# Performance work log

Measured on AMD Instinct MI355X. Metric: run time of the kernel, lower is better.

Reference implementation:

```python
import jax, jax.numpy as jnp
import numpy as np

EPS = 1e-5
K = 20

def knn_idx(x, k):
    # x: (B, C, N); returns indices of k nearest neighbors (incl. self), (B, N, k)
    xx = jnp.sum(x * x, axis=1, keepdims=True)            # (B,1,N)
    inner = -2.0 * jnp.einsum('bcn,bcm->bnm', x, x)       # (B,N,N)
    d = -jnp.swapaxes(xx, 1, 2) - inner - xx              # -||xi - xj||^2
    return jax.lax.top_k(d, k)[1]

def graph_feature(x, k):
    # x: (B, C, N) -> (B, 2C, N, k) with [neighbor - center, center]
    B, C, N = x.shape
    idx = knn_idx(x, k)                                   # (B,N,k)
    feat = jnp.swapaxes(x, 1, 2)                          # (B,N,C)
    nb = jax.vmap(lambda f, i: f[i])(feat, idx)           # (B,N,k,C) gather
    ctr = jnp.broadcast_to(feat[:, :, None, :], nb.shape)
    out = jnp.concatenate([nb - ctr, ctr], axis=-1)       # (B,N,k,2C)
    return jnp.transpose(out, (0, 3, 1, 2))

def bn(x, g, b, m, v):
    # inference-mode batchnorm over channel axis 1
    shape = (1, -1) + (1,) * (x.ndim - 2)
    inv = g / jnp.sqrt(v + EPS)
    return x * inv.reshape(shape) + (b - m * inv).reshape(shape)

def edge_block(x, W, g, b, m, v):
    f = graph_feature(x, K)                               # (B,2C,N,k)
    h = jnp.einsum('bcnk,oc->bonk', f, W)                 # 1x1 conv, no bias
    h = jax.nn.relu(bn(h, g, b, m, v))
    return jnp.max(h, axis=-1)                            # max over k -> (B,O,N)

def _forward(x, W1, W2, W3, W4, W5,
             g1, b1, m1, v1, g2, b2, m2, v2, g3, b3, m3, v3,
             g4, b4, m4, v4, g5, b5, m5, v5, g6, b6, m6, v6,
             g7, b7, m7, v7, L1W, L2W, L2b, L3W, L3b):
    x1 = edge_block(x, W1, g1, b1, m1, v1)                # (B,64,N)
    x2 = edge_block(x1, W2, g2, b2, m2, v2)               # (B,64,N)
    x3 = edge_block(x2, W3, g3, b3, m3, v3)               # (B,128,N)
    x4 = edge_block(x3, W4, g4, b4, m4, v4)               # (B,256,N)
    cat = jnp.concatenate([x1, x2, x3, x4], axis=1)       # (B,512,N)
    h = jnp.einsum('bcn,oc->bon', cat, W5)                # conv5 1x1
    h = jax.nn.relu(bn(h, g5, b5, m5, v5))
    h = jnp.max(h, axis=-1)                               # adaptive max pool -> (B,1024)
    h = jax.nn.relu(bn(h @ L1W.T, g6, b6, m6, v6))        # dropout = identity (eval)
    h = jax.nn.relu(bn(h @ L2W.T + L2b, g7, b7, m7, v7))
    return h @ L3W.T + L3b                                # (B, num_classes)

def _bn_params(keys, c):
    k0, k1, k2, k3 = keys
    g = jax.random.uniform(k0, (c,), jnp.float32, 0.5, 1.5)
    b = 0.1 * jax.random.normal(k1, (c,), jnp.float32)
    m = 0.1 * jax.random.normal(k2, (c,), jnp.float32)
    v = jax.random.uniform(k3, (c,), jnp.float32, 0.5, 1.5)
    return g, b, m, v

def setup_inputs() -> dict:
    key = jax.random.key(0)
    ks = jax.random.split(key, 40)
    d = {}
    d['x'] = jax.random.normal(ks[0], (8, 4, 1024), jnp.float32)
    def w(k, o, i):
        return jax.random.normal(k, (o, i), jnp.float32) * np.float32(np.sqrt(2.0 / i))
    d['W1'] = w(ks[1], 64, 8)
    d['W2'] = w(ks[2], 64, 128)
    d['W3'] = w(ks[3], 128, 128)
    d['W4'] = w(ks[4], 256, 256)
    d['W5'] = w(ks[5], 1024, 512)
    for i, c in enumerate([64, 64, 128, 256, 1024, 512, 256]):
        g, b, m, v = _bn_params(jax.random.split(ks[6 + i], 4), c)
        d[f'g{i+1}'], d[f'b{i+1}'], d[f'm{i+1}'], d[f'v{i+1}'] = g, b, m, v
    d['L1W'] = w(ks[20], 512, 1024)
    d['L2W'] = w(ks[21], 256, 512)
    d['L2b'] = 0.1 * jax.random.normal(ks[22], (256,), jnp.float32)
    d['L3W'] = w(ks[23], 8, 256)
    d['L3b'] = 0.1 * jax.random.normal(ks[24], (8,), jnp.float32)
    return d

def reference(x, W1, W2, W3, W4, W5,
              g1, b1, m1, v1, g2, b2, m2, v2, g3, b3, m3, v3,
              g4, b4, m4, v4, g5, b5, m5, v5, g6, b6, m6, v6,
              g7, b7, m7, v7, L1W, L2W, L2b, L3W, L3b):
    return _forward(x, W1, W2, W3, W4, W5,
                    g1, b1, m1, v1, g2, b2, m2, v2, g3, b3, m3, v3,
                    g4, b4, m4, v4, g5, b5, m5, v5, g6, b6, m6, v6,
                    g7, b7, m7, v7, L1W, L2W, L2b, L3W, L3b)
```

## Files before the change

### kernel.cpp

```cpp
#include <hip/hip_runtime.h>
#include <cstdint>

#define BB 8
#define NN 1024
#define KK 20
#define EPSV 1e-5f

typedef __attribute__((ext_vector_type(8))) short bf16x8;
typedef __attribute__((ext_vector_type(4))) float f32x4;

__device__ __forceinline__ unsigned fenc(float f) {
  unsigned u = __float_as_uint(f);
  return (u & 0x80000000u) ? ~u : (u | 0x80000000u);
}
__device__ __forceinline__ float fdec(unsigned u) {
  u = (u & 0x80000000u) ? (u & 0x7FFFFFFFu) : ~u;
  return __uint_as_float(u);
}
__device__ __forceinline__ unsigned short f2bf(float f) {
  unsigned u = __float_as_uint(f);
  unsigned r = u + 0x7FFFu + ((u >> 16) & 1u);
  return (unsigned short)(r >> 16);
}
__device__ __forceinline__ unsigned mbcnt64(unsigned long long m) {
  unsigned r = __builtin_amdgcn_mbcnt_lo((unsigned)m, 0u);
  return __builtin_amdgcn_mbcnt_hi((unsigned)(m >> 32), r);
}

template<int C>
__global__ __launch_bounds__(256) void xx_kernel(const float* __restrict__ x, float* __restrict__ xx) {
  int p = blockIdx.x * 256 + threadIdx.x;
  if (p >= BB * NN) return;
  int b = p >> 10, n = p & (NN - 1);
  const float* xb = x + (size_t)b * C * NN + n;
  float s = 0.f;
  #pragma unroll
  for (int c = 0; c < C; ++c) { float t = xb[(size_t)c * NN]; s = fmaf(t, t, s); }
  xx[p] = s;
}

template<int C>
__global__ __launch_bounds__(256) void dist_kernel(const float* __restrict__ x, const float* __restrict__ xx,
                                                   float* __restrict__ d, int b0) {
  constexpr int CC = (C < 32) ? C : 32;
  __shared__ __align__(16) float xi[CC][128];
  __shared__ __align__(16) float xj[CC][64];
  int bl = blockIdx.z, b = b0 + bl;
  int i0 = blockIdx.y * 128, j0 = blockIdx.x * 64;
  int t = threadIdx.x;
  int tj = t & 15, ti = t >> 4;
  float acc[8][4] = {};
  const float* xb = x + (size_t)b * C * NN;
  for (int c0 = 0; c0 < C; c0 += CC) {
    __syncthreads();
    for (int p = t; p < CC * 32; p += 256) {
      int cc = p >> 5, col = (p & 31) * 4;
      *reinterpret_cast<float4*>(&xi[cc][col]) =
        *reinterpret_cast<const float4*>(&xb[(size_t)(c0 + cc) * NN + i0 + col]);
    }
    for (int p = t; p < CC * 16; p += 256) {
      int cc = p >> 4, col = (p & 15) * 4;
      *reinterpret_cast<float4*>(&xj[cc][col]) =
        *reinterpret_cast<const float4*>(&xb[(size_t)(c0 + cc) * NN + j0 + col]);
    }
    __syncthreads();
    #pragma unroll
    for (int cc = 0; cc < CC; ++cc) {
      float4 A0 = *reinterpret_cast<const float4*>(&xi[cc][ti * 8]);
      float4 A1 = *reinterpret_cast<const float4*>(&xi[cc][ti * 8 + 4]);
      float4 Bv = *reinterpret_cast<const float4*>(&xj[cc][tj * 4]);
      float av[8] = {A0.x, A0.y, A0.z, A0.w, A1.x, A1.y, A1.z, A1.w};
      float bv[4] = {Bv.x, Bv.y, Bv.z, Bv.w};
      #pragma unroll
      for (int a = 0; a < 8; ++a)
        #pragma unroll
        for (int q = 0; q < 4; ++q)
          acc[a][q] = fmaf(av[a], bv[q], acc[a][q]);
    }
  }
  float xxj[4];
  #pragma unroll
  for (int q = 0; q < 4; ++q) xxj[q] = xx[b * NN + j0 + tj * 4 + q];
  #pragma unroll
  for (int a = 0; a < 8; ++a) {
    int i = i0 + ti * 8 + a;
    float xxi = xx[b * NN + i];
    float4 o;
    o.x = 2.f * acc[a][0] - xxi - xxj[0];
    o.y = 2.f * acc[a][1] - xxi - xxj[1];
    o.z = 2.f * acc[a][2] - xxi - xxj[2];
    o.w = 2.f * acc[a][3] - xxi - xxj[3];
    *reinterpret_cast<float4*>(&d[((size_t)bl * NN + i) * NN + j0 + tj * 4]) = o;
  }
}

__global__ __launch_bounds__(256) void topk_kernel(const float* __restrict__ d, int* __restrict__ idx, int b0) {
  int t = threadIdx.x;
  int wave = t >> 6, lane = t & 63;
  int bl = blockIdx.y, b = b0 + bl;
  int i = blockIdx.x * 4 + wave;
  const float* row = d + ((size_t)bl * NN + i) * NN;

  unsigned v[16];
  #pragma unroll
  for (int p = 0; p < 4; ++p) {
    float4 f = *reinterpret_cast<const float4*>(&row[p * 256 + lane * 4]);
    v[p * 4 + 0] = fenc(f.x);
    v[p * 4 + 1] = fenc(f.y);
    v[p * 4 + 2] = fenc(f.z);
    v[p * 4 + 3] = fenc(f.w);
  }

  unsigned long long lo = 0, hi = 0xFFFFFFFFull;
  while (lo < hi) {
    unsigned long long mid = lo + ((hi - lo + 1) >> 1);
    unsigned mt = (unsigned)mid;
    int c = 0;
    #pragma unroll
    for (int e = 0; e < 16; ++e)
      c += __popcll(__ballot(v[e] >= mt));
    if (c >= KK) lo = mid; else hi = mid - 1;
  }
  unsigned T = (unsigned)lo;

  int* op = idx + ((size_t)b * NN + i) * KK;
  int base = 0, n1 = 0;
  #pragma unroll
  for (int e = 0; e < 16; ++e) {
    unsigned long long mask = __ballot(v[e] > T);
    unsigned mb = mbcnt64(mask);
    if (v[e] > T) op[base + mb] = (e >> 2) * 256 + lane * 4 + (e & 3);
    base += __popcll(mask);
  }
  n1 = base;
  int need = KK - n1;
  int neq = 0;
  #pragma unroll
  for (int e = 0; e < 16; ++e) neq += __popcll(__ballot(v[e] == T));
  if (neq == need) {
    #pragma unroll
    for (int e = 0; e < 16; ++e) {
      unsigned long long mask = __ballot(v[e] == T);
      unsigned mb = mbcnt64(mask);
      if (v[e] == T) op[base + mb] = (e >> 2) * 256 + lane * 4 + (e & 3);
      base += __popcll(mask);
    }
  } else {
    unsigned taken = 0;
    for (int s = 0; s < need; ++s) {
      int jm = 1 << 30;
      #pragma unroll
      for (int e = 0; e < 16; ++e) {
        if (v[e] == T && !((taken >> e) & 1u)) {
          int j = (e >> 2) * 256 + lane * 4 + (e & 3);
          jm = jm < j ? jm : j;
        }
      }
      #pragma unroll
      for (int st = 1; st < 64; st <<= 1) {
        int oj = __shfl_xor(jm, st);
        jm = jm < oj ? jm : oj;
      }
      if (lane == ((jm >> 2) & 63)) {
        int e = (((jm >> 8) << 2) | (jm & 3));
        taken |= 1u << e;
        op[base + s] = jm;
      }
    }
  }
}

template<int C, int O>
__global__ __launch_bounds__(256) void pgemm_kernel(const float* __restrict__ x, const float* __restrict__ W,
                                                    float* __restrict__ Plo, float* __restrict__ Phi) {
  constexpr int CC = (C < 64) ? C : 64;
  __shared__ __align__(16) float xs[CC][64];
  __shared__ __align__(16) float wls[CC][68];
  __shared__ __align__(16) float whs[CC][68];
  int b = blockIdx.z;
  int o0 = blockIdx.y * 64, n0 = blockIdx.x * 64;
  int t = threadIdx.x;
  int tn = t & 15, to = t >> 4;
  float accl[4][4] = {}, acch[4][4] = {};
  const float* xb = x + (size_t)b * C * NN;
  for (int c0 = 0; c0 < C; c0 += CC) {
    __syncthreads();
    for (int p = t; p < CC * 64; p += 256) {
      int cc = p >> 6, col = p & 63;
      xs[cc][col] = xb[(size_t)(c0 + cc) * NN + n0 + col];
    }
    for (int p = t; p < 64 * CC; p += 256) {
      int ol = p / CC, cc = p % CC;
      wls[cc][ol] = W[(size_t)(o0 + ol) * (2 * C) + c0 + cc];
      whs[cc][ol] = W[(size_t)(o0 + ol) * (2 * C) + C + c0 + cc];
    }
    __syncthreads();
    #pragma unroll
    for (int cc = 0; cc < CC; ++cc) {
      float4 X  = *reinterpret_cast<const float4*>(&xs[cc][tn * 4]);
      float4 Wl = *reinterpret_cast<const float4*>(&wls[cc][to * 4]);
      float4 Wh = *reinterpret_cast<const float4*>(&whs[cc][to * 4]);
      float xv[4] = {X.x, X.y, X.z, X.w};
      float wl[4] = {Wl.x, Wl.y, Wl.z, Wl.w};
      float wh[4] = {Wh.x, Wh.y, Wh.z, Wh.w};
      #pragma unroll
      for (int a = 0; a < 4; ++a)
        #pragma unroll
        for (int q = 0; q < 4; ++q) {
          accl[a][q] = fmaf(wl[a], xv[q], accl[a][q]);
          acch[a][q] = fmaf(wh[a], xv[q], acch[a][q]);
        }
    }
  }
  #pragma unroll
  for (int a = 0; a < 4; ++a) {
    int o = o0 + to * 4 + a;
    size_t base = ((size_t)b * O + o) * NN + n0 + tn * 4;
    float4 vl = {accl[a][0], accl[a][1], accl[a][2], accl[a][3]};
    float4 vh = {acch[a][0], acch[a][1], acch[a][2], acch[a][3]};
    *reinterpret_cast<float4*>(&Plo[base]) = vl;
    *reinterpret_cast<float4*>(&Phi[base]) = vh;
  }
}

__global__ __launch_bounds__(256) void edgemax_kernel(const float* __restrict__ Plo, const float* __restrict__ Phi,
    const int* __restrict__ idx, const float* __restrict__ g, const float* __restrict__ bt,
    const float* __restrict__ m, const float* __restrict__ v,
    float* __restrict__ xout, int O) {
  __shared__ __align__(16) float srow[2][NN];
  __shared__ __align__(16) float sphi[2][64];
  __shared__ int   sidx[64 * KK];
  __shared__ float sinv[32], ssb[32];
  int b = blockIdx.z, n0 = blockIdx.y * 64, o0 = blockIdx.x * 32;
  int t = threadIdx.x;
  if (t < 32) {
    float inv = g[o0 + t] / sqrtf(v[o0 + t] + EPSV);
    sinv[t] = inv; ssb[t] = bt[o0 + t] - m[o0 + t] * inv;
  }
  for (int p = t; p < 64 * KK; p += 256) sidx[p] = idx[((size_t)b * NN + n0) * KK + p];
  const float* plobase = Plo + (size_t)b * O * NN;
  const float* phibase = Phi + (size_t)b * O * NN;
  float4 cur0 = *reinterpret_cast<const float4*>(&plobase[(size_t)(o0 + 0) * NN + t * 4]);
  float4 cur1 = *reinterpret_cast<const float4*>(&plobase[(size_t)(o0 + 1) * NN + t * 4]);
  float4 curphi;
  if (t < 32) curphi = *reinterpret_cast<const float4*>(&phibase[(size_t)(o0 + (t >> 4)) * NN + n0 + (t & 15) * 4]);
  __syncthreads();
  int n = t >> 2, kg = t & 3;
  int j0 = sidx[n * KK + kg * 5 + 0];
  int j1 = sidx[n * KK + kg * 5 + 1];
  int j2 = sidx[n * KK + kg * 5 + 2];
  int j3 = sidx[n * KK + kg * 5 + 3];
  int j4 = sidx[n * KK + kg * 5 + 4];
  for (int oo = 0; oo < 32; oo += 2) {
    *reinterpret_cast<float4*>(&srow[0][t * 4]) = cur0;
    *reinterpret_cast<float4*>(&srow[1][t * 4]) = cur1;
    if (t < 32) *reinterpret_cast<float4*>(&sphi[t >> 4][(t & 15) * 4]) = curphi;
    if (oo < 30) {
      cur0 = *reinterpret_cast<const float4*>(&plobase[(size_t)(o0 + oo + 2) * NN + t * 4]);
      cur1 = *reinterpret_cast<const float4*>(&plobase[(size_t)(o0 + oo + 3) * NN + t * 4]);
      if (t < 32) curphi = *reinterpret_cast<const float4*>(&phibase[(size_t)(o0 + oo + 2 + (t >> 4)) * NN + n0 + (t & 15) * 4]);
    }
    __syncthreads();
    float mx0 = srow[0][j0];
    mx0 = fmaxf(mx0, srow[0][j1]);
    mx0 = fmaxf(mx0, srow[0][j2]);
    mx0 = fmaxf(mx0, srow[0][j3]);
    mx0 = fmaxf(mx0, srow[0][j4]);
    float mx1 = srow[1][j0];
    mx1 = fmaxf(mx1, srow[1][j1]);
    mx1 = fmaxf(mx1, srow[1][j2]);
    mx1 = fmaxf(mx1, srow[1][j3]);
    mx1 = fmaxf(mx1, srow[1][j4]);
    mx0 = fmaxf(mx0, __shfl_xor(mx0, 1));
    mx0 = fmaxf(mx0, __shfl_xor(mx0, 2));
    mx1 = fmaxf(mx1, __shfl_xor(mx1, 1));
    mx1 = fmaxf(mx1, __shfl_xor(mx1, 2));
    if (kg == 0) {
      float z0 = mx0 - srow[0][n0 + n] + sphi[0][n];
      float z1 = mx1 - srow[1][n0 + n] + sphi[1][n];
      xout[((size_t)b * O + o0 + oo) * NN + n0 + n]     = fmaxf(fmaf(z0, sinv[oo],     ssb[oo]),     0.f);
      xout[((size_t)b * O + o0 + oo + 1) * NN + n0 + n] = fmaxf(fmaf(z1, sinv[oo + 1], ssb[oo + 1]), 0.f);
    }
    __syncthreads();
  }
}

__global__ __launch_bounds__(256) void tcvt_kernel(const float* __restrict__ src,
    unsigned short* __restrict__ dst, int Csrc, int c0) {
  __shared__ float tile[64][65];
  int b = blockIdx.z, cb = blockIdx.y * 64, n0 = blockIdx.x * 64;
  int t = threadIdx.x;
  const float* s = src + ((size_t)b * Csrc + cb) * NN + n0;
  #pragma unroll
  for (int rr = 0; rr < 4; ++rr) {
    int r = (t >> 4) + rr * 16;
    float4 v = *reinterpret_cast<const float4*>(&s[(size_t)r * NN + (t & 15) * 4]);
    tile[r][(t & 15) * 4 + 0] = v.x;
    tile[r][(t & 15) * 4 + 1] = v.y;
    tile[r][(t & 15) * 4 + 2] = v.z;
    tile[r][(t & 15) * 4 + 3] = v.w;
  }
  __syncthreads();
  #pragma unroll
  for (int rr = 0; rr < 2; ++rr) {
    int chunk = t + 256 * rr;
    int n = chunk >> 3, cg = (chunk & 7) * 8;
    unsigned short u[8];
    #pragma unroll
    for (int j = 0; j < 8; ++j) u[j] = f2bf(tile[cg + j][n]);
    *reinterpret_cast<uint4*>(&dst[((size_t)b * NN + n0 + n) * 512 + c0 + cb + cg]) =
      *reinterpret_cast<const uint4*>(u);
  }
}

__global__ __launch_bounds__(256) void cvtw_kernel(const float* __restrict__ W, unsigned short* __restrict__ Wb) {
  int p = (blockIdx.x * 256 + threadIdx.x) * 4;
  float4 v = *reinterpret_cast<const float4*>(&W[p]);
  unsigned short u[4] = {f2bf(v.x), f2bf(v.y), f2bf(v.z), f2bf(v.w)};
  *reinterpret_cast<uint2*>(&Wb[p]) = *reinterpret_cast<const uint2*>(u);
}

__global__ __launch_bounds__(256) void pgemm4_mfma_kernel(const unsigned short* __restrict__ Xb,
    const unsigned short* __restrict__ W4b, float* __restrict__ Plo_t, float* __restrict__ Phi_t) {
  int b = blockIdx.z;
  int n0 = blockIdx.x * 128, o0 = blockIdx.y * 64;
  int t = threadIdx.x, lane = t & 63, w = t >> 6;
  int r = lane & 15, kc = lane >> 4;
  const unsigned short* A  = Xb + ((size_t)b * NN + n0 + w * 32 + r) * 512 + 128 + kc * 8;
  const unsigned short* Bw = W4b + ((size_t)(o0 + r)) * 256 + kc * 8;
  f32x4 accl0[4] = {}, accl1[4] = {}, acch0[4] = {}, acch1[4] = {};
  #pragma unroll
  for (int ks = 0; ks < 128; ks += 32) {
    bf16x8 a0 = *reinterpret_cast<const bf16x8*>(A + ks);
    bf16x8 a1 = *reinterpret_cast<const bf16x8*>(A + 16 * 512 + ks);
    #pragma unroll
    for (int j = 0; j < 4; ++j) {
      bf16x8 bl = *reinterpret_cast<const bf16x8*>(Bw + (size_t)j * 16 * 256 + ks);
      bf16x8 bh = *reinterpret_cast<const bf16x8*>(Bw + (size_t)j * 16 * 256 + 128 + ks);
      accl0[j] = __builtin_amdgcn_mfma_f32_16x16x32_bf16(a0, bl, accl0[j], 0, 0, 0);
      accl1[j] = __builtin_amdgcn_mfma_f32_16x16x32_bf16(a1, bl, accl1[j], 0, 0, 0);
      acch0[j] = __builtin_amdgcn_mfma_f32_16x16x32_bf16(a0, bh, acch0[j], 0, 0, 0);
      acch1[j] = __builtin_amdgcn_mfma_f32_16x16x32_bf16(a1, bh, acch1[j], 0, 0, 0);
    }
  }
  #pragma unroll
  for (int j = 0; j < 4; ++j) {
    #pragma unroll
    for (int reg = 0; reg < 4; ++reg) {
      size_t n_a = (size_t)b * NN + n0 + w * 32 + kc * 4 + reg;
      size_t n_b = n_a + 16;
      int oc = o0 + j * 16 + r;
      Plo_t[n_a * 256 + oc] = accl0[j][reg];
      Plo_t[n_b * 256 + oc] = accl1[j][reg];
      Phi_t[n_a * 256 + oc] = acch0[j][reg];
      Phi_t[n_b * 256 + oc] = acch1[j][reg];
    }
  }
}

__global__ __launch_bounds__(256) void edgemax4_kernel(const float* __restrict__ Plo_t,
    const float* __restrict__ Phi_t, const int* __restrict__ idx,
    const float* __restrict__ g, const float* __restrict__ bt,
    const float* __restrict__ m, const float* __restrict__ v,
    unsigned short* __restrict__ Xb) {
  int b = blockIdx.y, t = threadIdx.x;
  int n = blockIdx.x * 4 + (t >> 6);
  int oc = (t & 63) * 4;
  const int* ip = idx + ((size_t)b * NN + n) * KK;
  const float* base = Plo_t + (size_t)b * NN * 256;
  float4 mx = {-3.4e38f, -3.4e38f, -3.4e38f, -3.4e38f};
  #pragma unroll
  for (int k = 0; k < KK; ++k) {
    float4 vv = *reinterpret_cast<const float4*>(base + (size_t)ip[k] * 256 + oc);
    mx.x = fmaxf(mx.x, vv.x);
    mx.y = fmaxf(mx.y, vv.y);
    mx.z = fmaxf(mx.z, vv.z);
    mx.w = fmaxf(mx.w, vv.w);
  }
  float4 self = *reinterpret_cast<const float4*>(base + (size_t)n * 256 + oc);
  float4 ph = *reinterpret_cast<const float4*>(Phi_t + ((size_t)b * NN + n) * 256 + oc);
  float4 gg = *reinterpret_cast<const float4*>(g + oc);
  float4 bb = *reinterpret_cast<const float4*>(bt + oc);
  float4 mm = *reinterpret_cast<const float4*>(m + oc);
  float4 vv4 = *reinterpret_cast<const float4*>(v + oc);
  float mxa[4] = {mx.x, mx.y, mx.z, mx.w};
  float sfa[4] = {self.x, self.y, self.z, self.w};
  float pha[4] = {ph.x, ph.y, ph.z, ph.w};
  float ga[4] = {gg.x, gg.y, gg.z, gg.w};
  float ba[4] = {bb.x, bb.y, bb.z, bb.w};
  float ma[4] = {mm.x, mm.y, mm.z, mm.w};
  float va[4] = {vv4.x, vv4.y, vv4.z, vv4.w};
  unsigned short u[4];
  #pragma unroll
  for (int e = 0; e < 4; ++e) {
    float inv = ga[e] / sqrtf(va[e] + EPSV);
    float z = mxa[e] - sfa[e] + pha[e];
    float y = fmaxf(fmaf(z, inv, ba[e] - ma[e] * inv), 0.f);
    u[e] = f2bf(y);
  }
  *reinterpret_cast<uint2*>(&Xb[((size_t)b * NN + n) * 512 + 256 + oc]) =
    *reinterpret_cast<const uint2*>(u);
}

__global__ __launch_bounds__(256, 1) void conv5_mfma_kernel(const unsigned short* __restrict__ Xb,
    const unsigned short* __restrict__ W5b, unsigned* __restrict__ henc) {
  __shared__ __align__(16) unsigned short lA[4096 * 8];
  int b = blockIdx.z;
  int n0 = blockIdx.x * 128, o0 = blockIdx.y * 64;
  int t = threadIdx.x, lane = t & 63, w = t >> 6;
  int r = lane & 15, kc = lane >> 4;

  const unsigned short* B = Xb + ((size_t)b * NN + n0 + w * 32 + r) * 512 + kc * 8;
  bf16x8 b0[16], b1[16];
  #pragma unroll
  for (int ks = 0; ks < 16; ++ks) {
    b0[ks] = *reinterpret_cast<const bf16x8*>(B + ks * 32);
    b1[ks] = *reinterpret_cast<const bf16x8*>(B + 16 * 512 + ks * 32);
  }

  #pragma unroll
  for (int i = 0; i < 16; ++i) {
    int e = i * 256 + t;
    int le = e & 63, je = (e >> 6) & 3, kse = e >> 8;
    const unsigned short* src = W5b + ((size_t)(o0 + je * 16 + (le & 15))) * 512 + ((le >> 4) & 3) * 8 + kse * 32;
    *reinterpret_cast<uint4*>(&lA[(size_t)e * 8]) = *reinterpret_cast<const uint4*>(src);
  }
  __syncthreads();

  f32x4 acc00 = {}, acc01 = {}, acc10 = {}, acc11 = {};
  f32x4 acc20 = {}, acc21 = {}, acc30 = {}, acc31 = {};
  #pragma unroll
  for (int ks = 0; ks < 16; ++ks) {
    bf16x8 a0 = *reinterpret_cast<const bf16x8*>(&lA[(size_t)((ks * 4 + 0) * 64 + lane) * 8]);
    bf16x8 a1 = *reinterpret_cast<const bf16x8*>(&lA[(size_t)((ks * 4 + 1) * 64 + lane) * 8]);
    bf16x8 a2 = *reinterpret_cast<const bf16x8*>(&lA[(size_t)((ks * 4 + 2) * 64 + lane) * 8]);
    bf16x8 a3 = *reinterpret_cast<const bf16x8*>(&lA[(size_t)((ks * 4 + 3) * 64 + lane) * 8]);
    acc00 = __builtin_amdgcn_mfma_f32_16x16x32_bf16(a0, b0[ks], acc00, 0, 0, 0);
    acc01 = __builtin_amdgcn_mfma_f32_16x16x32_bf16(a0, b1[ks], acc01, 0, 0, 0);
    acc10 = __builtin_amdgcn_mfma_f32_16x16x32_bf16(a1, b0[ks], acc10, 0, 0, 0);
    acc11 = __builtin_amdgcn_mfma_f32_16x16x32_bf16(a1, b1[ks], acc11, 0, 0, 0);
    acc20 = __builtin_amdgcn_mfma_f32_16x16x32_bf16(a2, b0[ks], acc20, 0, 0, 0);
    acc21 = __builtin_amdgcn_mfma_f32_16x16x32_bf16(a2, b1[ks], acc21, 0, 0, 0);
    acc30 = __builtin_amdgcn_mfma_f32_16x16x32_bf16(a3, b0[ks], acc30, 0, 0, 0);
    acc31 = __builtin_amdgcn_mfma_f32_16x16x32_bf16(a3, b1[ks], acc31, 0, 0, 0);
  }

  f32x4 m0 = {fmaxf(acc00[0], acc01[0]), fmaxf(acc00[1], acc01[1]),
              fmaxf(acc00[2], acc01[2]), fmaxf(acc00[3], acc01[3])};
  f32x4 m1 = {fmaxf(acc10[0], acc11[0]), fmaxf(acc10[1], acc11[1]),
              fmaxf(acc10[2], acc11[2]), fmaxf(acc10[3], acc11[3])};
  f32x4 m2 = {fmaxf(acc20[0], acc21[0]), fmaxf(acc20[1], acc21[1]),
              fmaxf(acc20[2], acc21[2]), fmaxf(acc20[3], acc21[3])};
  f32x4 m3 = {fmaxf(acc30[0], acc31[0]), fmaxf(acc30[1], acc31[1]),
              fmaxf(acc30[2], acc31[2]), fmaxf(acc30[3], acc31[3])};
  #pragma unroll
  for (int st = 1; st < 16; st <<= 1) {
    #pragma unroll
    for (int reg = 0; reg < 4; ++reg) {
      m0[reg] = fmaxf(m0[reg], __shfl_xor(m0[reg], st));
      m1[reg] = fmaxf(m1[reg], __shfl_xor(m1[reg], st));
      m2[reg] = fmaxf(m2[reg], __shfl_xor(m2[reg], st));
      m3[reg] = fmaxf(m3[reg], __shfl_xor(m3[reg], st));
    }
  }
  if (r == 0) {
    #pragma unroll
    for (int reg = 0; reg < 4; ++reg) {
      atomicMax(&henc[b * 1024 + o0 + 0 * 16 + kc * 4 + reg], fenc(m0[reg]));
      atomicMax(&henc[b * 1024 + o0 + 1 * 16 + kc * 4 + reg], fenc(m1[reg]));
      atomicMax(&henc[b * 1024 + o0 + 2 * 16 + kc * 4 + reg], fenc(m2[reg]));
      atomicMax(&henc[b * 1024 + o0 + 3 * 16 + kc * 4 + reg], fenc(m3[reg]));
    }
  }
}

__global__ __launch_bounds__(256) void fc1_kernel(
    const unsigned* __restrict__ henc,
    const float* __restrict__ g5, const float* __restrict__ b5, const float* __restrict__ m5, const float* __restrict__ v5,
    const float* __restrict__ L1W,
    const float* __restrict__ g6, const float* __restrict__ b6, const float* __restrict__ m6, const float* __restrict__ v6,
    float* __restrict__ y1) {
  __shared__ float sh[1024];
  int b = blockIdx.y, t = threadIdx.x;
  int o0 = blockIdx.x * 64;
  for (int o = t; o < 1024; o += 256) {
    float f = fdec(henc[b * 1024 + o]);
    float inv = g5[o] / sqrtf(v5[o] + EPSV);
    sh[o] = fmaxf(fmaf(f, inv, b5[o] - m5[o] * inv), 0.f);
  }
  __syncthreads();
  int o = o0 + (t >> 2), part = t & 3;
  float acc = 0.f;
  const float4* w4 = reinterpret_cast<const float4*>(L1W + (size_t)o * 1024 + part * 256);
  const float4* h4 = reinterpret_cast<const float4*>(sh + part * 256);
  #pragma unroll 8
  for (int c = 0; c < 64; ++c) {
    float4 a = w4[c], q = h4[c];
    acc = fmaf(a.x, q.x, fmaf(a.y, q.y, fmaf(a.z, q.z, fmaf(a.w, q.w, acc))));
  }
  acc += __shfl_xor(acc, 1);
  acc += __shfl_xor(acc, 2);
  if (part == 0) {
    float inv = g6[o] / sqrtf(v6[o] + EPSV);
    y1[b * 512 + o] = fmaxf(fmaf(acc, inv, b6[o] - m6[o] * inv), 0.f);
  }
}

__global__ __launch_bounds__(256) void fc2_kernel(
    const float* __restrict__ y1,
    const float* __restrict__ L2W, const float* __restrict__ L2b,
    const float* __restrict__ g7, const float* __restrict__ b7, const float* __restrict__ m7, const float* __restrict__ v7,
    const float* __restrict__ L3W, const float* __restrict__ L3b,
    float* __restrict__ out) {
  __shared__ float sy1[512];
  __shared__ float sy2[256];
  int b = blockIdx.x, t = threadIdx.x;
  for (int o = t; o < 512; o += 256) sy1[o] = y1[b * 512 + o];
  __syncthreads();
  {
    int o = t;
    float acc = L2b[o];
    const float4* w4 = reinterpret_cast<const float4*>(L2W + (size_t)o * 512);
    const float4* q4 = reinterpret_cast<const float4*>(sy1);
    for (int c = 0; c < 128; ++c) {
      float4 a = w4[c], q = q4[c];
      acc = fmaf(a.x, q.x, fmaf(a.y, q.y, fmaf(a.z, q.z, fmaf(a.w, q.w, acc))));
    }
    float inv = g7[o] / sqrtf(v7[o] + EPSV);
    sy2[o] = fmaxf(fmaf(acc, inv, b7[o] - m7[o] * inv), 0.f);
  }
  __syncthreads();
  if (t < 8) {
    float acc = L3b[t];
    const float4* w4 = reinterpret_cast<const float4*>(L3W + (size_t)t * 256);
    const float4* q4 = reinterpret_cast<const float4*>(sy2);
    for (int c = 0; c < 64; ++c) {
      float4 a = w4[c], q = q4[c];
      acc = fmaf(a.x, q.x, fmaf(a.y, q.y, fmaf(a.z, q.z, fmaf(a.w, q.w, acc))));
    }
    out[b * 8 + t] = acc;
  }
}

extern "C" void kernel_launch(void* const* d_in, const int* in_sizes, int n_in,
                              void* d_out, int out_size, void* d_ws, size_t ws_size,
                              hipStream_t stream) {
  (void)in_sizes; (void)n_in; (void)out_size;
  const float* x   = (const float*)d_in[0];
  const float* W1  = (const float*)d_in[1];
  const float* W2  = (const float*)d_in[2];
  const float* W3  = (const float*)d_in[3];
  const float* W4  = (const float*)d_in[4];
  const float* W5  = (const float*)d_in[5];
  const float* bnp[7][4];
  for (int i = 0; i < 7; ++i)
    for (int j = 0; j < 4; ++j)
      bnp[i][j] = (const float*)d_in[6 + i * 4 + j];
  const float* L1W = (const float*)d_in[34];
  const float* L2W = (const float*)d_in[35];
  const float* L2b = (const float*)d_in[36];
  const float* L3W = (const float*)d_in[37];
  const float* L3b = (const float*)d_in[38];
  float* out = (float*)d_out;

  char* wsb = (char*)d_ws;
  size_t off = 0;
  auto alloc = [&](size_t bytes) -> void* {
    void* p = wsb + off; off += (bytes + 255) & ~(size_t)255; return p;
  };
  int*      idx  = (int*)     alloc((size_t)BB * NN * KK * 4);
  float*    xx   = (float*)   alloc((size_t)BB * NN * 4);
  float*    x1   = (float*)   alloc((size_t)BB * 64  * NN * 4);
  float*    x2   = (float*)   alloc((size_t)BB * 64  * NN * 4);
  float*    x3   = (float*)   alloc((size_t)BB * 128 * NN * 4);
  float*    Plo  = (float*)   alloc((size_t)BB * 256 * NN * 4);
  float*    Phi  = (float*)   alloc((size_t)BB * 256 * NN * 4);
  unsigned* henc = (unsigned*)alloc((size_t)BB * 1024 * 4);
  float*    y1   = (float*)   alloc((size_t)BB * 512 * 4);
  unsigned short* Xb  = (unsigned short*)alloc((size_t)BB * NN * 512 * 2);
  unsigned short* W5b = (unsigned short*)alloc((size_t)1024 * 512 * 2);
  unsigned short* W4b = (unsigned short*)alloc((size_t)256 * 256 * 2);
  size_t left = (ws_size > off) ? (ws_size - off) : 0;
  int nb = 8;
  while (nb > 1 && (size_t)nb * NN * NN * 4 > left) nb >>= 1;
  float* dbuf = (float*)(wsb + off);

  dim3 thr(256);
  #define KNN_PHASE(CIN, XIN)                                                              \
    xx_kernel<CIN><<<dim3(32), thr, 0, stream>>>(XIN, xx);                                 \
    for (int b0 = 0; b0 < BB; b0 += nb) {                                                  \
      dist_kernel<CIN><<<dim3(16, 8, nb), thr, 0, stream>>>(XIN, xx, dbuf, b0);            \
      topk_kernel<<<dim3(NN / 4, nb), thr, 0, stream>>>(dbuf, idx, b0);                    \
    }

  cvtw_kernel<<<dim3(512), thr, 0, stream>>>(W5, W5b);
  cvtw_kernel<<<dim3(64), thr, 0, stream>>>(W4, W4b);

  KNN_PHASE(4, x)
  pgemm_kernel<4, 64><<<dim3(16, 1, BB), thr, 0, stream>>>(x, W1, Plo, Phi);
  edgemax_kernel<<<dim3(2, 16, BB), thr, 0, stream>>>(Plo, Phi, idx,
      bnp[0][0], bnp[0][1], bnp[0][2], bnp[0][3], x1, 64);
  tcvt_kernel<<<dim3(16, 1, BB), thr, 0, stream>>>(x1, Xb, 64, 0);
  KNN_PHASE(64, x1)
  pgemm_kernel<64, 64><<<dim3(16, 1, BB), thr, 0, stream>>>(x1, W2, Plo, Phi);
  edgemax_kernel<<<dim3(2, 16, BB), thr, 0, stream>>>(Plo, Phi, idx,
      bnp[1][0], bnp[1][1], bnp[1][2], bnp[1][3], x2, 64);
  tcvt_kernel<<<dim3(16, 1, BB), thr, 0, stream>>>(x2, Xb, 64, 64);
  KNN_PHASE(64, x2)
  pgemm_kernel<64, 128><<<dim3(16, 2, BB), thr, 0, stream>>>(x2, W3, Plo, Phi);
  edgemax_kernel<<<dim3(4, 16, BB), thr, 0, stream>>>(Plo, Phi, idx,
      bnp[2][0], bnp[2][1], bnp[2][2], bnp[2][3], x3, 128);
  tcvt_kernel<<<dim3(16, 2, BB), thr, 0, stream>>>(x3, Xb, 128, 128);
  KNN_PHASE(128, x3)
  pgemm4_mfma_kernel<<<dim3(8, 4, BB), thr, 0, stream>>>(Xb, W4b, Plo, Phi);
  edgemax4_kernel<<<dim3(256, BB), thr, 0, stream>>>(Plo, Phi, idx,
      bnp[3][0], bnp[3][1], bnp[3][2], bnp[3][3], Xb);
  #undef KNN_PHASE

  hipMemsetAsync(henc, 0, (size_t)BB * 1024 * 4, stream);
  conv5_mfma_kernel<<<dim3(8, 16, BB), thr, 0, stream>>>(Xb, W5b, henc);

  fc1_kernel<<<dim3(8, BB), thr, 0, stream>>>(henc,
      bnp[4][0], bnp[4][1], bnp[4][2], bnp[4][3], L1W,
      bnp[5][0], bnp[5][1], bnp[5][2], bnp[5][3], y1);
  fc2_kernel<<<dim3(BB), thr, 0, stream>>>(y1,
      L2W, L2b, bnp[6][0], bnp[6][1], bnp[6][2], bnp[6][3], L3W, L3b, out);
}
```

Before: 425.4 us.

## Enlarge dist tile to 128x128 with double-buffered direct-to-LDS loads

The pairwise-distance kernel now computes a 128x128 output tile per block, with each thread holding an 8x8 accumulator instead of 8x4. This halves the grid and raises arithmetic intensity per LDS read. Channel chunks are double-buffered in LDS and loaded with global_load_lds, so the next chunk's fetch overlaps the current chunk's FMAs. The cost is more registers per thread and fewer blocks, which may hurt occupancy, and the kernel is only part of the total runtime.

```diff
diff --git a/kernel.cpp b/kernel.cpp
--- a/kernel.cpp
+++ b/kernel.cpp
@@ -25,6 +25,11 @@
 __device__ __forceinline__ unsigned mbcnt64(unsigned long long m) {
   unsigned r = __builtin_amdgcn_mbcnt_lo((unsigned)m, 0u);
   return __builtin_amdgcn_mbcnt_hi((unsigned)(m >> 32), r);
+}
+__device__ __forceinline__ void gload_lds16(const float* g, float* l) {
+  __builtin_amdgcn_global_load_lds(
+      (const __attribute__((address_space(1))) void*)g,
+      (__attribute__((address_space(3))) void*)l, 16, 0, 0);
 }
 
 template<int C>
@@ -43,54 +48,73 @@
 __global__ __launch_bounds__(256) void dist_kernel(const float* __restrict__ x, const float* __restrict__ xx,
                                                    float* __restrict__ d, int b0) {
   constexpr int CC = (C < 32) ? C : 32;
-  __shared__ __align__(16) float xi[CC][128];
-  __shared__ __align__(16) float xj[CC][64];
+  constexpr int NI = CC * 32;
+  constexpr int NU = (NI + 255) / 256;
+  __shared__ __align__(16) float xi[2][CC][128];
+  __shared__ __align__(16) float xj[2][CC][128];
   int bl = blockIdx.z, b = b0 + bl;
-  int i0 = blockIdx.y * 128, j0 = blockIdx.x * 64;
+  int i0 = blockIdx.y * 128, j0 = blockIdx.x * 128;
   int t = threadIdx.x;
-  int tj = t & 15, ti = t >> 4;
-  float acc[8][4] = {};
+  int w = t >> 6, lane = t & 63;
+  int wi = (w >> 1) * 64, wj = (w & 1) * 64;
+  int li = (lane >> 3) * 8, lj = (lane & 7) * 8;
+  float acc[8][8] = {};
   const float* xb = x + (size_t)b * C * NN;
+
+  auto stage = [&](int buf, int c0) {
+    float* bi = &xi[buf][0][0];
+    float* bj = &xj[buf][0][0];
+    #pragma unroll
+    for (int u = 0; u < NU; ++u) {
+      int p = u * 256 + t;
+      if (p < NI) {
+        gload_lds16(&xb[(size_t)(c0 + (p >> 5)) * NN + i0 + (p & 31) * 4], bi + p * 4);
+        gload_lds16(&xb[(size_t)(c0 + (p >> 5)) * NN + j0 + (p & 31) * 4], bj + p * 4);
+      }
+    }
+  };
+
+  stage(0, 0);
+  __syncthreads();
+  int cur = 0;
   for (int c0 = 0; c0 < C; c0 += CC) {
-    __syncthreads();
-    for (int p = t; p < CC * 32; p += 256) {
-      int cc = p >> 5, col = (p & 31) * 4;
-      *reinterpret_cast<float4*>(&xi[cc][col]) =
-        *reinterpret_cast<const float4*>(&xb[(size_t)(c0 + cc) * NN + i0 + col]);
-    }
-    for (int p = t; p < CC * 16; p += 256) {
-      int cc = p >> 4, col = (p & 15) * 4;
-      *reinterpret_cast<float4*>(&xj[cc][col]) =
-        *reinterpret_cast<const float4*>(&xb[(size_t)(c0 + cc) * NN + j0 + col]);
-    }
-    __syncthreads();
+    if (c0 + CC < C) stage(cur ^ 1, c0 + CC);
     #pragma unroll
     for (int cc = 0; cc < CC; ++cc) {
-      float4 A0 = *reinterpret_cast<const float4*>(&xi[cc][ti * 8]);
-      float4 A1 = *reinterpret_cast<const float4*>(&xi[cc][ti * 8 + 4]);
-      float4 Bv = *reinterpret_cast<const float4*>(&xj[cc][tj * 4]);
+      float4 A0 = *reinterpret_cast<const float4*>(&xi[cur][cc][wi + li]);
+      float4 A1 = *reinterpret_cast<const float4*>(&xi[cur][cc][wi + li + 4]);
+      float4 B0 = *reinterpret_cast<const float4*>(&xj[cur][cc][wj + lj]);
+      float4 B1 = *reinterpret_cast<const float4*>(&xj[cur][cc][wj + lj + 4]);
       float av[8] = {A0.x, A0.y, A0.z, A0.w, A1.x, A1.y, A1.z, A1.w};
-      float bv[4] = {Bv.x, Bv.y, Bv.z, Bv.w};
+      float bv[8] = {B0.x, B0.y, B0.z, B0.w, B1.x, B1.y, B1.z, B1.w};
       #pragma unroll
       for (int a = 0; a < 8; ++a)
         #pragma unroll
-        for (int q = 0; q < 4; ++q)
+        for (int q = 0; q < 8; ++q)
           acc[a][q] = fmaf(av[a], bv[q], acc[a][q]);
     }
-  }
-  float xxj[4];
-  #pragma unroll
-  for (int q = 0; q < 4; ++q) xxj[q] = xx[b * NN + j0 + tj * 4 + q];
+    __syncthreads();
+    cur ^= 1;
+  }
+
+  float xxj[8];
+  #pragma unroll
+  for (int q = 0; q < 8; ++q) xxj[q] = xx[b * NN + j0 + wj + lj + q];
   #pragma unroll
   for (int a = 0; a < 8; ++a) {
-    int i = i0 + ti * 8 + a;
+    int i = i0 + wi + li + a;
     float xxi = xx[b * NN + i];
-    float4 o;
-    o.x = 2.f * acc[a][0] - xxi - xxj[0];
-    o.y = 2.f * acc[a][1] - xxi - xxj[1];
-    o.z = 2.f * acc[a][2] - xxi - xxj[2];
-    o.w = 2.f * acc[a][3] - xxi - xxj[3];
-    *reinterpret_cast<float4*>(&d[((size_t)bl * NN + i) * NN + j0 + tj * 4]) = o;
+    float4 o0v, o1v;
+    o0v.x = 2.f * acc[a][0] - xxi - xxj[0];
+    o0v.y = 2.f * acc[a][1] - xxi - xxj[1];
+    o0v.z = 2.f * acc[a][2] - xxi - xxj[2];
+    o0v.w = 2.f * acc[a][3] - xxi - xxj[3];
+    o1v.x = 2.f * acc[a][4] - xxi - xxj[4];
+    o1v.y = 2.f * acc[a][5] - xxi - xxj[5];
+    o1v.z = 2.f * acc[a][6] - xxi - xxj[6];
+    o1v.w = 2.f * acc[a][7] - xxi - xxj[7];
+    *reinterpret_cast<float4*>(&d[((size_t)bl * NN + i) * NN + j0 + wj + lj]) = o0v;
+    *reinterpret_cast<float4*>(&d[((size_t)bl * NN + i) * NN + j0 + wj + lj + 4]) = o1v;
   }
 }
 
@@ -589,7 +613,7 @@
   #define KNN_PHASE(CIN, XIN)                                                              \
     xx_kernel<CIN><<<dim3(32), thr, 0, stream>>>(XIN, xx);                                 \
     for (int b0 = 0; b0 < BB; b0 += nb) {                                                  \
-      dist_kernel<CIN><<<dim3(16, 8, nb), thr, 0, stream>>>(XIN, xx, dbuf, b0);            \
+      dist_kernel<CIN><<<dim3(8, 8, nb), thr, 0, stream>>>(XIN, xx, dbuf, b0);             \
       topk_kernel<<<dim3(NN / 4, nb), thr, 0, stream>>>(dbuf, idx, b0);                    \
     }
 
```

Result: slower. 480.0 us (+12.9%).
